# Performance work log

Measured on AMD Instinct MI355X. Metric: run time of the kernel, lower is better.

Reference implementation:

```python
import jax, jax.numpy as jnp
import numpy as np

N, T, F, H, NH, OUT = 4096, 32, 7, 64, 8, 8


def setup_inputs() -> dict:
    key = jax.random.key(0)
    ks = jax.random.split(key, 24)
    def nrm(k, shape, scale):
        return jax.random.normal(k, shape, jnp.float32) * scale
    s_gru = 1.0 / np.sqrt(H)
    s_gat = 1.0 / np.sqrt(NH * OUT)
    s_lin = 0.05
    return {
        "inputs": jax.random.normal(ks[0], (N, T, F), jnp.float32),
        "adj": jax.random.randint(ks[1], (N, N), 0, 2, jnp.int32),
        "W_ih": nrm(ks[2], (3 * H, F), s_gru),
        "W_hh": nrm(ks[3], (3 * H, H), s_gru),
        "b_ih": nrm(ks[4], (3 * H,), s_gru),
        "b_hh": nrm(ks[5], (3 * H,), s_gru),
        "gat_w": nrm(ks[6], (H, NH * OUT), s_gat),
        "gat_wu": nrm(ks[7], (NH, OUT, 1), 1.0),
        "gat_wv": nrm(ks[8], (NH, OUT, 1), 1.0),
        "gat_bias": nrm(ks[9], (1, NH * OUT), s_gat),
        "proj_w": nrm(ks[10], (NH * OUT, H), s_lin),
        "proj_b": nrm(ks[11], (NH * OUT,), s_lin),
        "mlp_self_w": nrm(ks[12], (H, H), s_lin),
        "mlp_self_b": nrm(ks[13], (H,), s_lin),
        "mlp_pos_w": nrm(ks[14], (H, NH * OUT), s_lin),
        "mlp_pos_b": nrm(ks[15], (H,), s_lin),
        "sem_w1": nrm(ks[16], (H, H), s_lin),
        "sem_b1": nrm(ks[17], (H,), s_lin),
        "sem_w2": nrm(ks[18], (1, H), s_lin),
        "pred_w": nrm(ks[19], (1, H), s_lin),
        "pred_b": nrm(ks[20], (1,), s_lin),
    }


def reference(inputs, adj, W_ih, W_hh, b_ih, b_hh, gat_w, gat_wu, gat_wv,
              gat_bias, proj_w, proj_b, mlp_self_w, mlp_self_b,
              mlp_pos_w, mlp_pos_b, sem_w1, sem_b1, sem_w2, pred_w, pred_b):
    n = inputs.shape[0]
    # --- GRU encoder (batch_first, 1 layer); take final hidden state ---
    gx = jnp.einsum('ntf,gf->tng', inputs, W_ih) + b_ih  # [T, N, 3H]
    h0 = jnp.zeros((n, W_hh.shape[1]), inputs.dtype)

    def step(h, g):
        gh = h @ W_hh.T + b_hh
        gxr, gxz, gxn = jnp.split(g, 3, axis=-1)
        ghr, ghz, ghn = jnp.split(gh, 3, axis=-1)
        r = jax.nn.sigmoid(gxr + ghr)
        z = jax.nn.sigmoid(gxz + ghz)
        nn_ = jnp.tanh(gxn + r * ghn)
        return (1.0 - z) * nn_ + z * h, None

    h, _ = jax.lax.scan(step, h0, gx)  # [N, H]

    # --- multi-head GAT over dense adjacency ---
    sup = (h @ gat_w).reshape(n, NH, OUT).transpose(1, 0, 2)  # [nh, N, out]
    f1 = jnp.einsum('hnd,hdo->hn', sup, gat_wu)[:, None, :]   # [nh, 1, N]
    f2 = jnp.einsum('hnd,hdo->hn', sup, gat_wv)[:, :, None]   # [nh, N, 1]
    logits = jax.nn.leaky_relu(f1 + f2, negative_slope=0.2)   # [nh, N, N]
    adjf = adj.astype(logits.dtype)[None]                     # [1, N, N]
    mw = logits * adjf
    ex = jnp.exp(mw - jnp.max(mw, axis=2, keepdims=True)) * (adjf > 0)
    attn = ex / jnp.clip(jnp.sum(ex, axis=2, keepdims=True), 1e-10)
    pos = jnp.einsum('hij,hjd->hid', attn, sup)               # [nh, N, out]
    pos = pos.transpose(1, 0, 2).reshape(n, NH * OUT)
    pos = pos + gat_bias + h @ proj_w.T + proj_b              # bias + residual proj

    # --- stack self/pos channels, PairNorm (mode='PN') ---
    s = jnp.stack([h @ mlp_self_w.T + mlp_self_b,
                   pos @ mlp_pos_w.T + mlp_pos_b], axis=1)    # [N, 2, H]
    s = s - s.mean(axis=0)
    rownorm_mean = jnp.sqrt(1e-6 + jnp.mean(jnp.sum(s * s, axis=1)))
    s = s / rownorm_mean

    # --- semantic attention over the 2 channels ---
    w = jnp.tanh(s @ sem_w1.T + sem_b1) @ sem_w2.T            # [N, 2, 1]
    we = jnp.exp(w - jnp.max(w, axis=1, keepdims=True))
    beta = we / (jnp.sum(we, axis=1, keepdims=True) + 1e-10)
    emb = jnp.sum(beta * s, axis=1)                           # [N, H]

    # --- predictor ---
    return jax.nn.sigmoid(emb @ pred_w.T + pred_b)            # [N, 1]
```

## Files before the change

kernel.cpp:

```cpp
#include <hip/hip_runtime.h>
#include <math.h>

#define NN 4096
#define TT 32
#define FF 7
#define HH 64
#define NHEAD 8
#define DOUT 8
#define LOG2E 1.44269504f

#if __has_builtin(__builtin_amdgcn_exp2f)
#define EXP2(x) __builtin_amdgcn_exp2f(x)
#else
#define EXP2(x) exp2f(x)
#endif

typedef short bf16x8 __attribute__((ext_vector_type(8)));
typedef float f32x4 __attribute__((ext_vector_type(4)));

__device__ __forceinline__ float sigm(float x){
  x = fminf(fmaxf(x, -30.f), 30.f);
  return 1.f / (1.f + __expf(-x));
}
__device__ __forceinline__ float tanh_fast(float x){
  x = fminf(fmaxf(x, -15.f), 15.f);
  float e = __expf(2.f*x);
  return (e - 1.f) / (e + 1.f);
}
__device__ __forceinline__ unsigned short bf16rne(float f){
  unsigned u = __float_as_uint(f);
  u += 0x7fffu + ((u >> 16) & 1u);
  return (unsigned short)(u >> 16);
}
__device__ __forceinline__ unsigned bfpack2(float a, float b){
  return (unsigned)bf16rne(a) | ((unsigned)bf16rne(b) << 16);
}
__device__ __forceinline__ unsigned cvtpk_bf16(float a, float b){
  unsigned r;
  asm("v_cvt_pk_bf16_f32 %0, %1, %2" : "=v"(r) : "v"(a), "v"(b));
  return r;
}

__global__ __launch_bounds__(256) void k0_prep(
    const float* __restrict__ pw, const float* __restrict__ msw,
    const float* __restrict__ mpw, const float* __restrict__ sw1,
    const float* __restrict__ Wih, const float* __restrict__ Whh,
    const float* __restrict__ bih, const float* __restrict__ bhh,
    float* __restrict__ wtproj, float* __restrict__ wtself,
    float* __restrict__ wtpos, float* __restrict__ wtsem,
    uint4* __restrict__ whhF, uint4* __restrict__ wihF)
{
  if (blockIdx.x < 16){
    int tid = threadIdx.x + blockIdx.x*256;
    int d = tid >> 6, k = tid & 63;
    wtproj[k*64+d] = pw[tid];
    wtself[k*64+d] = msw[tid];
    wtpos[k*64+d]  = mpw[tid];
    wtsem[k*64+d]  = sw1[tid];
    return;
  }
  int idx = (blockIdx.x-16)*256 + threadIdx.x;
  if (idx < 24*64){
    int f = idx >> 6, lane = idx & 63;
    int T = f >> 1, c = f & 1;
    int g = T*16 + (lane & 15);
    const float* wp = Whh + g*64 + c*32 + (lane >> 4)*8;
    uint4 v;
    v.x = bfpack2(wp[0], wp[1]);
    v.y = bfpack2(wp[2], wp[3]);
    v.z = bfpack2(wp[4], wp[5]);
    v.w = bfpack2(wp[6], wp[7]);
    whhF[idx] = v;
  } else if (idx < 36*64){
    int i2 = idx - 24*64;
    int T = i2 >> 6, lane = i2 & 63;
    int g = T*16 + (lane & 15);
    int kg = lane >> 4;
    float bias = (T < 8) ? (bih[g] + bhh[g]) : bih[g];
    float f8[8];
    #pragma unroll
    for (int j = 0; j < 8; ++j){
      int k = kg*8 + j;
      f8[j] = (k < 7) ? Wih[g*7 + k] : ((k == 7) ? bias : 0.f);
    }
    uint4 v;
    v.x = bfpack2(f8[0], f8[1]); v.y = bfpack2(f8[2], f8[3]);
    v.z = bfpack2(f8[4], f8[5]); v.w = bfpack2(f8[6], f8[7]);
    wihF[i2] = v;
  }
}

__global__ __launch_bounds__(256) void k1_gru(
    const float* __restrict__ x,
    const uint4* __restrict__ whhF,
    const uint4* __restrict__ wihF,
    const float* __restrict__ bhh,
    float* __restrict__ hout)
{
  __shared__ __align__(16) short s_xb[32][16][8];
  __shared__ __align__(16) short s_hb[2][16][72];

  int tid = threadIdx.x;
  int lane = tid & 63, w = tid >> 6;
  int nb = blockIdx.x * 16;
  int row = lane & 15;
  int kg  = lane >> 4;

  union U { bf16x8 v; uint4 q; };
  U u;
  u.q = wihF[w*64 + lane];           bf16x8 fRx  = u.v;
  u.q = whhF[(w*2+0)*64 + lane];     bf16x8 fRh0 = u.v;
  u.q = whhF[(w*2+1)*64 + lane];     bf16x8 fRh1 = u.v;
  u.q = wihF[(4+w)*64 + lane];       bf16x8 fZx  = u.v;
  u.q = whhF[((4+w)*2+0)*64 + lane]; bf16x8 fZh0 = u.v;
  u.q = whhF[((4+w)*2+1)*64 + lane]; bf16x8 fZh1 = u.v;
  u.q = wihF[(8+w)*64 + lane];       bf16x8 fNx  = u.v;
  u.q = whhF[((8+w)*2+0)*64 + lane]; bf16x8 fNh0 = u.v;
  u.q = whhF[((8+w)*2+1)*64 + lane]; bf16x8 fNh1 = u.v;

  for (int s = tid; s < 4096; s += 256){
    int t = s >> 7, node = (s >> 3) & 15, k = s & 7;
    float v = (k < 7) ? x[(size_t)(nb + node)*224 + t*7 + k] : ((k == 7) ? 1.f : 0.f);
    s_xb[t][node][k] = (short)bf16rne(v);
  }
  for (int i = tid; i < 576; i += 256) ((unsigned*)&s_hb[0][0][0])[i] = 0u;

  float bhn_[4];
  #pragma unroll
  for (int j = 0; j < 4; ++j) bhn_[j] = bhh[128 + w*16 + kg*4 + j];
  float hreg[4] = {0.f, 0.f, 0.f, 0.f};
  f32x4 z4 = {0.f, 0.f, 0.f, 0.f};

  __syncthreads();
  int cur = 0;
  for (int t = 0; t < TT; ++t){
    bf16x8 bx = {0,0,0,0,0,0,0,0};
    if (lane < 16) bx = *(const bf16x8*)&s_xb[t][row][0];
    bf16x8 bh0 = *(const bf16x8*)&s_hb[cur][row][kg*8];
    bf16x8 bh1 = *(const bf16x8*)&s_hb[cur][row][32 + kg*8];

    f32x4 aR = __builtin_amdgcn_mfma_f32_16x16x32_bf16(fRx, bx, z4, 0, 0, 0);
    aR = __builtin_amdgcn_mfma_f32_16x16x32_bf16(fRh0, bh0, aR, 0, 0, 0);
    aR = __builtin_amdgcn_mfma_f32_16x16x32_bf16(fRh1, bh1, aR, 0, 0, 0);
    f32x4 aZ = __builtin_amdgcn_mfma_f32_16x16x32_bf16(fZx, bx, z4, 0, 0, 0);
    aZ = __builtin_amdgcn_mfma_f32_16x16x32_bf16(fZh0, bh0, aZ, 0, 0, 0);
    aZ = __builtin_amdgcn_mfma_f32_16x16x32_bf16(fZh1, bh1, aZ, 0, 0, 0);
    f32x4 aNx = __builtin_amdgcn_mfma_f32_16x16x32_bf16(fNx, bx, z4, 0, 0, 0);
    f32x4 aNh = __builtin_amdgcn_mfma_f32_16x16x32_bf16(fNh0, bh0, z4, 0, 0, 0);
    aNh = __builtin_amdgcn_mfma_f32_16x16x32_bf16(fNh1, bh1, aNh, 0, 0, 0);

    #pragma unroll
    for (int j = 0; j < 4; ++j){
      float rr = sigm(aR[j]);
      float zz = sigm(aZ[j]);
      float nn = tanh_fast(aNx[j] + rr*(aNh[j] + bhn_[j]));
      hreg[j] = (1.f - zz)*nn + zz*hreg[j];
    }
    uint2 p;
    p.x = bfpack2(hreg[0], hreg[1]);
    p.y = bfpack2(hreg[2], hreg[3]);
    *(uint2*)&s_hb[cur^1][row][w*16 + kg*4] = p;
    __syncthreads();
    cur ^= 1;
  }

  #pragma unroll
  for (int j = 0; j < 4; ++j)
    hout[(size_t)(nb + row)*64 + w*16 + kg*4 + j] = hreg[j];
}

__global__ __launch_bounds__(256) void k2_sup(
    const float* __restrict__ h, const float* __restrict__ gat_w,
    const float* __restrict__ wu, const float* __restrict__ wv,
    unsigned short* __restrict__ supbJ,
    float* __restrict__ f1t,
    float* __restrict__ f2)
{
  int tid = threadIdx.x;
  int wave = tid >> 6, lane = tid & 63;
  int n = blockIdx.x*4 + wave;
  float hreg = h[n*64 + lane];
  float acc = 0.f;
  #pragma unroll
  for (int k = 0; k < 64; ++k){
    float hk = __shfl(hreg, k, 64);
    acc += hk * gat_w[k*64 + lane];
  }
  int hh = lane >> 3, o = lane & 7;
  supbJ[(size_t)hh*32768 + (n>>3)*64 + o*8 + (n&7)] = bf16rne(acc);
  float p1 = acc * wu[lane];
  float p2 = acc * wv[lane];
  #pragma unroll
  for (int s = 1; s < 8; s <<= 1){
    p1 += __shfl_xor(p1, s, 64);
    p2 += __shfl_xor(p2, s, 64);
  }
  if (o == 0){
    f1t[(size_t)hh*NN + n] = p1 * LOG2E;
    f2[n*8 + hh] = p2 * LOG2E;
  }
}

__global__ __launch_bounds__(256) void k2c_pack(const int* __restrict__ adj,
                                               unsigned long long* __restrict__ adjmT)
{
  int lane = threadIdx.x & 63, wave = threadIdx.x >> 6;
  int row = blockIdx.x*4 + wave;
  const int* ap = adj + (size_t)row*NN;
  size_t base = (size_t)(row >> 4)*1024 + (row & 15);
  #pragma unroll 8
  for (int s = 0; s < 64; ++s){
    unsigned long long m = __ballot(ap[s*64 + lane] != 0);
    if (lane == 0) adjmT[base + s*16] = m;
  }
}

__global__ __launch_bounds__(256) void k3_gat(
    const unsigned long long* __restrict__ adjmT,
    const unsigned short* __restrict__ supbJ,
    const float* __restrict__ f1t,
    const float* __restrict__ f2,
    float* __restrict__ posg)
{
  __shared__ f32x4 s_acc[4][64];
  int tid = threadIdx.x;
  int lane = tid & 63, js = tid >> 6;
  int gid = blockIdx.x;
  int ib = gid >> 3, h = gid & 7;
  int i0 = ib*16;
  int col = lane & 15;
  int kg  = lane >> 4;

  float f2v = f2[(size_t)(i0+col)*8 + h];

  const unsigned long long* mrowT = adjmT + (size_t)ib*1024;
  const float* f1p = f1t + (size_t)h*NN;
  const unsigned short* bsrcJ = supbJ + (size_t)h*32768;
  unsigned bge8 = (col >= 8) ? 0xffffffffu : 0u;

  f32x4 acc = {0.f, 0.f, 0.f, 0.f};

  #pragma unroll 4
  for (int cc = 0; cc < 32; ++cc){
    int c = js*32 + cc;
    int j8 = c*32 + kg*8;
    unsigned long long mw = mrowT[(c >> 1)*16 + col];
    unsigned mb = (unsigned)(mw >> (((c & 1) << 5) + (kg << 3)));
    float4 fa = *(const float4*)(f1p + j8);
    float4 fb = *(const float4*)(f1p + j8 + 4);

    float p[8];
    p[0]=fa.x; p[1]=fa.y; p[2]=fa.z; p[3]=fa.w;
    p[4]=fb.x; p[5]=fb.y; p[6]=fb.z; p[7]=fb.w;
    #pragma unroll
    for (int e = 0; e < 8; ++e){
      float ls = p[e] + f2v;
      float lrs = fmaxf(ls, 0.2f*ls);
      float pe = EXP2(lrs);
      p[e] = (mb & (1u << e)) ? pe : 0.f;
    }
    union { bf16x8 v; unsigned u[4]; } A;
    A.u[0] = cvtpk_bf16(p[0], p[1]);
    A.u[1] = cvtpk_bf16(p[2], p[3]);
    A.u[2] = cvtpk_bf16(p[4], p[5]);
    A.u[3] = cvtpk_bf16(p[6], p[7]);

    union { bf16x8 v; unsigned u[4]; } B;
    uint4 ld = *(const uint4*)(bsrcJ + (size_t)(c*4 + kg)*64 + (col & 7)*8);
    B.u[0] = bge8 ? 0x3f803f80u : ld.x;
    B.u[1] = bge8 ? 0x3f803f80u : ld.y;
    B.u[2] = bge8 ? 0x3f803f80u : ld.z;
    B.u[3] = bge8 ? 0x3f803f80u : ld.w;

    acc = __builtin_amdgcn_mfma_f32_16x16x32_bf16(A.v, B.v, acc, 0, 0, 0);
  }

  s_acc[js][lane] = acc;
  __syncthreads();
  if (js == 0){
    f32x4 a1 = s_acc[1][lane], a2 = s_acc[2][lane], a3 = s_acc[3][lane];
    #pragma unroll
    for (int j = 0; j < 4; ++j) acc[j] += a1[j] + a2[j] + a3[j];

    int slane = (lane & 48) + 8;
    #pragma unroll
    for (int r4 = 0; r4 < 4; ++r4){
      float sv = __shfl(acc[r4], slane, 64);
      float inv = 1.f / fmaxf(sv, 1e-10f);
      if (col < 8)
        posg[(size_t)(i0 + kg*4 + r4)*64 + h*8 + col] = acc[r4] * inv;
    }
  }
}

__global__ __launch_bounds__(256) void k4_mix(
    const float* __restrict__ h, const float* __restrict__ posg,
    const float* __restrict__ gat_bias, const float* __restrict__ proj_b,
    const float* __restrict__ wtproj, const float* __restrict__ wtself,
    const float* __restrict__ wtpos,
    const float* __restrict__ mlp_self_b, const float* __restrict__ mlp_pos_b,
    float* __restrict__ s0, float* __restrict__ s1, float* __restrict__ part)
{
  int tid = threadIdx.x;
  int wave = tid >> 6, lane = tid & 63;
  int n = blockIdx.x*4 + wave;
  float hreg = h[n*64 + lane];
  float pr = proj_b[lane];
  float se = mlp_self_b[lane];
  #pragma unroll
  for (int k = 0; k < 64; ++k){
    float hk = __shfl(hreg, k, 64);
    pr += hk * wtproj[k*64 + lane];
    se += hk * wtself[k*64 + lane];
  }
  float posf = posg[n*64 + lane] + gat_bias[lane] + pr;
  float s1v = mlp_pos_b[lane];
  #pragma unroll
  for (int k = 0; k < 64; ++k){
    float pk = __shfl(posf, k, 64);
    s1v += pk * wtpos[k*64 + lane];
  }
  s0[n*64+lane] = se;
  s1[n*64+lane] = s1v;

  __shared__ float sb0[4][64];
  __shared__ float sb1[4][64];
  __shared__ float sq[4];
  sb0[wave][lane] = se;
  sb1[wave][lane] = s1v;
  float q = se*se + s1v*s1v;
  #pragma unroll
  for (int s = 1; s < 64; s <<= 1) q += __shfl_xor(q, s, 64);
  if (lane == 0) sq[wave] = q;
  __syncthreads();
  if (tid < 64){
    part[blockIdx.x*130 + tid] = sb0[0][tid]+sb0[1][tid]+sb0[2][tid]+sb0[3][tid];
  } else if (tid < 128){
    int d = tid - 64;
    part[blockIdx.x*130 + 64 + d] = sb1[0][d]+sb1[1][d]+sb1[2][d]+sb1[3][d];
  } else if (tid == 128){
    part[blockIdx.x*130 + 128] = sq[0]+sq[1]+sq[2]+sq[3];
  }
}

__global__ __launch_bounds__(1024) void k5_stats(const float* __restrict__ part, float* __restrict__ stats)
{
  int tid = threadIdx.x;
  __shared__ float s_mu[8][128];
  __shared__ float s_sq[8];
  int c = tid & 127, ch = tid >> 7;
  float a = 0.f;
  for (int b = ch*128; b < ch*128+128; ++b) a += part[b*130 + c];
  s_mu[ch][c] = a;
  if (tid < 8){
    float q = 0.f;
    for (int b = tid*128; b < tid*128+128; ++b) q += part[b*130 + 128];
    s_sq[tid] = q;
  }
  __syncthreads();
  if (tid < 128){
    float m = 0.f;
    #pragma unroll
    for (int j = 0; j < 8; ++j) m += s_mu[j][tid];
    s_mu[0][tid] = m;
    stats[tid] = m / 4096.f;
  }
  __syncthreads();
  if (tid == 0){
    float sq = 0.f;
    #pragma unroll
    for (int j = 0; j < 8; ++j) sq += s_sq[j];
    float mu2 = 0.f;
    for (int i = 0; i < 128; ++i){ float m = s_mu[0][i] / 4096.f; mu2 += m*m; }
    float msq = sq/(4096.f*64.f) - mu2/64.f;
    stats[128] = 1.f / sqrtf(1e-6f + msq);
  }
}

__global__ __launch_bounds__(256) void k6_sem(
    const float* __restrict__ s0, const float* __restrict__ s1,
    const float* __restrict__ stats, const float* __restrict__ wtsem,
    const float* __restrict__ sem_b1, const float* __restrict__ sem_w2,
    const float* __restrict__ pred_w, const float* __restrict__ pred_b,
    float* __restrict__ out)
{
  int tid = threadIdx.x;
  int wave = tid >> 6, lane = tid & 63;
  int n = blockIdx.x*4 + wave;
  float rinv = stats[128];
  float a0 = (s0[n*64+lane] - stats[lane]) * rinv;
  float a1 = (s1[n*64+lane] - stats[64+lane]) * rinv;
  float t0 = sem_b1[lane], t1 = t0;
  #pragma unroll
  for (int k = 0; k < 64; ++k){
    float w = wtsem[k*64 + lane];
    t0 += __shfl(a0, k, 64) * w;
    t1 += __shfl(a1, k, 64) * w;
  }
  t0 = tanh_fast(t0); t1 = tanh_fast(t1);
  float w2 = sem_w2[lane];
  float w0 = t0*w2, w1 = t1*w2;
  #pragma unroll
  for (int s = 1; s < 64; s <<= 1){
    w0 += __shfl_xor(w0, s, 64);
    w1 += __shfl_xor(w1, s, 64);
  }
  float mx = fmaxf(w0, w1);
  float e0 = __expf(w0 - mx), e1 = __expf(w1 - mx);
  float denom = e0 + e1 + 1e-10f;
  float b0 = e0/denom, b1 = e1/denom;
  float emb = b0*a0 + b1*a1;
  float pl = emb * pred_w[lane];
  #pragma unroll
  for (int s = 1; s < 64; s <<= 1) pl += __shfl_xor(pl, s, 64);
  if (lane == 0) out[n] = sigm(pl + pred_b[0]);
}

extern "C" void kernel_launch(void* const* d_in, const int* in_sizes, int n_in,
                              void* d_out, int out_size, void* d_ws, size_t ws_size,
                              hipStream_t stream)
{
  (void)in_sizes; (void)n_in; (void)out_size; (void)ws_size;
  const float* x         = (const float*)d_in[0];
  const int*   adj       = (const int*)d_in[1];
  const float* W_ih      = (const float*)d_in[2];
  const float* W_hh      = (const float*)d_in[3];
  const float* b_ih      = (const float*)d_in[4];
  const float* b_hh      = (const float*)d_in[5];
  const float* gat_w     = (const float*)d_in[6];
  const float* gat_wu    = (const float*)d_in[7];
  const float* gat_wv    = (const float*)d_in[8];
  const float* gat_bias  = (const float*)d_in[9];
  const float* proj_w    = (const float*)d_in[10];
  const float* proj_b    = (const float*)d_in[11];
  const float* mlp_self_w= (const float*)d_in[12];
  const float* mlp_self_b= (const float*)d_in[13];
  const float* mlp_pos_w = (const float*)d_in[14];
  const float* mlp_pos_b = (const float*)d_in[15];
  const float* sem_w1    = (const float*)d_in[16];
  const float* sem_b1    = (const float*)d_in[17];
  const float* sem_w2    = (const float*)d_in[18];
  const float* pred_w    = (const float*)d_in[19];
  const float* pred_b    = (const float*)d_in[20];
  float* out = (float*)d_out;
  float* ws  = (float*)d_ws;

  float* h     = ws + 0;
  unsigned short* supbJ = (unsigned short*)(ws + 262144);
  float* f1t   = ws + 524288;
  float* f2    = ws + 557056;
  float* posg  = ws + 589824;
  float* s0    = ws + 851968;
  float* s1    = ws + 1114112;
  unsigned long long* adjmT = (unsigned long long*)(ws + 851968);
  uint4* whhF = (uint4*)(ws + 1114112 + 200000);
  uint4* wihF = whhF + 24*64;
  float* part  = ws + 1376256;
  float* stats = ws + 1517576;
  float* wtproj= ws + 1517712;
  float* wtself= wtproj + 4096;
  float* wtpos = wtself + 4096;
  float* wtsem = wtpos  + 4096;

  k0_prep<<<25, 256, 0, stream>>>(proj_w, mlp_self_w, mlp_pos_w, sem_w1,
                                  W_ih, W_hh, b_ih, b_hh,
                                  wtproj, wtself, wtpos, wtsem, whhF, wihF);
  k1_gru<<<256, 256, 0, stream>>>(x, whhF, wihF, b_hh, h);
  k2_sup<<<1024, 256, 0, stream>>>(h, gat_w, gat_wu, gat_wv, supbJ, f1t, f2);
  k2c_pack<<<1024, 256, 0, stream>>>(adj, adjmT);
  k3_gat<<<2048, 256, 0, stream>>>(adjmT, supbJ, f1t, f2, posg);
  k4_mix<<<1024, 256, 0, stream>>>(h, posg, gat_bias, proj_b, wtproj, wtself, wtpos,
                                   mlp_self_b, mlp_pos_b, s0, s1, part);
  k5_stats<<<1, 1024, 0, stream>>>(part, stats);
  k6_sem<<<1024, 256, 0, stream>>>(s0, s1, stats, wtsem, sem_b1, sem_w2, pred_w, pred_b, out);
}
```

Measured before the change: 165.2 us.

## Factor GAT exponentials, shrink GRU blocks to 4 nodes, load ones tile from memory

The GAT inner loop no longer evaluates exp2 per edge. The per-source factors exp2(f1) and exp2(0.2*f1) are computed once in k2_sup, and the per-row factors once per lane, so each edge costs a compare, two selects and a multiply. The sign test of the leaky-relu argument is done against exp2(-f2), and the product of two exponentials can overflow or lose precision differently from a single exp2. The GRU kernel now processes 4 nodes per block over 1024 blocks instead of 16 nodes over 256, which raises parallelism but wastes 12 of 16 MFMA rows. The constant-ones B operand is now read from a small buffer filled by k0_prep instead of being selected per element.

```diff
diff --git a/kernel.cpp b/kernel.cpp
--- a/kernel.cpp
+++ b/kernel.cpp
@@ -48,7 +48,8 @@
     const float* __restrict__ bih, const float* __restrict__ bhh,
     float* __restrict__ wtproj, float* __restrict__ wtself,
     float* __restrict__ wtpos, float* __restrict__ wtsem,
-    uint4* __restrict__ whhF, uint4* __restrict__ wihF)
+    uint4* __restrict__ whhF, uint4* __restrict__ wihF,
+    unsigned* __restrict__ onesb)
 {
   if (blockIdx.x < 16){
     int tid = threadIdx.x + blockIdx.x*256;
@@ -59,6 +60,7 @@
     wtsem[k*64+d]  = sw1[tid];
     return;
   }
+  if (blockIdx.x == 16 && threadIdx.x < 32) onesb[threadIdx.x] = 0x3f803f80u;
   int idx = (blockIdx.x-16)*256 + threadIdx.x;
   if (idx < 24*64){
     int f = idx >> 6, lane = idx & 63;
@@ -97,12 +99,12 @@
     const float* __restrict__ bhh,
     float* __restrict__ hout)
 {
-  __shared__ __align__(16) short s_xb[32][16][8];
-  __shared__ __align__(16) short s_hb[2][16][72];
+  __shared__ __align__(16) short s_xb[32][4][8];
+  __shared__ __align__(16) short s_hb[2][4][72];
 
   int tid = threadIdx.x;
   int lane = tid & 63, w = tid >> 6;
-  int nb = blockIdx.x * 16;
+  int nb = blockIdx.x * 4;
   int row = lane & 15;
   int kg  = lane >> 4;
 
@@ -118,12 +120,12 @@
   u.q = whhF[((8+w)*2+0)*64 + lane]; bf16x8 fNh0 = u.v;
   u.q = whhF[((8+w)*2+1)*64 + lane]; bf16x8 fNh1 = u.v;
 
-  for (int s = tid; s < 4096; s += 256){
-    int t = s >> 7, node = (s >> 3) & 15, k = s & 7;
+  for (int s = tid; s < 1024; s += 256){
+    int t = s >> 5, node = (s >> 3) & 3, k = s & 7;
     float v = (k < 7) ? x[(size_t)(nb + node)*224 + t*7 + k] : ((k == 7) ? 1.f : 0.f);
     s_xb[t][node][k] = (short)bf16rne(v);
   }
-  for (int i = tid; i < 576; i += 256) ((unsigned*)&s_hb[0][0][0])[i] = 0u;
+  for (int i = tid; i < 288; i += 256) ((unsigned*)&s_hb[0][0][0])[i] = 0u;
 
   float bhn_[4];
   #pragma unroll
@@ -133,11 +135,12 @@
 
   __syncthreads();
   int cur = 0;
+  int nrow = row & 3;
   for (int t = 0; t < TT; ++t){
     bf16x8 bx = {0,0,0,0,0,0,0,0};
-    if (lane < 16) bx = *(const bf16x8*)&s_xb[t][row][0];
-    bf16x8 bh0 = *(const bf16x8*)&s_hb[cur][row][kg*8];
-    bf16x8 bh1 = *(const bf16x8*)&s_hb[cur][row][32 + kg*8];
+    if (lane < 16) bx = *(const bf16x8*)&s_xb[t][nrow][0];
+    bf16x8 bh0 = *(const bf16x8*)&s_hb[cur][nrow][kg*8];
+    bf16x8 bh1 = *(const bf16x8*)&s_hb[cur][nrow][32 + kg*8];
 
     f32x4 aR = __builtin_amdgcn_mfma_f32_16x16x32_bf16(fRx, bx, z4, 0, 0, 0);
     aR = __builtin_amdgcn_mfma_f32_16x16x32_bf16(fRh0, bh0, aR, 0, 0, 0);
@@ -156,24 +159,28 @@
       float nn = tanh_fast(aNx[j] + rr*(aNh[j] + bhn_[j]));
       hreg[j] = (1.f - zz)*nn + zz*hreg[j];
     }
-    uint2 p;
-    p.x = bfpack2(hreg[0], hreg[1]);
-    p.y = bfpack2(hreg[2], hreg[3]);
-    *(uint2*)&s_hb[cur^1][row][w*16 + kg*4] = p;
+    if (row < 4){
+      uint2 p;
+      p.x = bfpack2(hreg[0], hreg[1]);
+      p.y = bfpack2(hreg[2], hreg[3]);
+      *(uint2*)&s_hb[cur^1][row][w*16 + kg*4] = p;
+    }
     __syncthreads();
     cur ^= 1;
   }
 
-  #pragma unroll
-  for (int j = 0; j < 4; ++j)
-    hout[(size_t)(nb + row)*64 + w*16 + kg*4 + j] = hreg[j];
+  if (row < 4){
+    #pragma unroll
+    for (int j = 0; j < 4; ++j)
+      hout[(size_t)(nb + row)*64 + w*16 + kg*4 + j] = hreg[j];
+  }
 }
 
 __global__ __launch_bounds__(256) void k2_sup(
     const float* __restrict__ h, const float* __restrict__ gat_w,
     const float* __restrict__ wu, const float* __restrict__ wv,
     unsigned short* __restrict__ supbJ,
-    float* __restrict__ f1t,
+    float2* __restrict__ e1t,
     float* __restrict__ f2)
 {
   int tid = threadIdx.x;
@@ -196,7 +203,8 @@
     p2 += __shfl_xor(p2, s, 64);
   }
   if (o == 0){
-    f1t[(size_t)hh*NN + n] = p1 * LOG2E;
+    float p1s = p1 * LOG2E;
+    e1t[(size_t)hh*NN + n] = make_float2(EXP2(p1s), EXP2(0.2f*p1s));
     f2[n*8 + hh] = p2 * LOG2E;
   }
 }
@@ -218,8 +226,9 @@
 __global__ __launch_bounds__(256) void k3_gat(
     const unsigned long long* __restrict__ adjmT,
     const unsigned short* __restrict__ supbJ,
-    const float* __restrict__ f1t,
+    const float2* __restrict__ e1t,
     const float* __restrict__ f2,
+    const unsigned short* __restrict__ onesb,
     float* __restrict__ posg)
 {
   __shared__ f32x4 s_acc[4][64];
@@ -231,12 +240,16 @@
   int col = lane & 15;
   int kg  = lane >> 4;
 
-  float f2v = f2[(size_t)(i0+col)*8 + h];
+  float f2s = f2[(size_t)(i0+col)*8 + h];
+  float E2  = EXP2(f2s);
+  float E2s = EXP2(0.2f*f2s);
+  float T   = EXP2(-f2s);
 
   const unsigned long long* mrowT = adjmT + (size_t)ib*1024;
-  const float* f1p = f1t + (size_t)h*NN;
-  const unsigned short* bsrcJ = supbJ + (size_t)h*32768;
-  unsigned bge8 = (col >= 8) ? 0xffffffffu : 0u;
+  const float2* e1p = e1t + (size_t)h*NN;
+  int bge8 = (col >= 8);
+  const unsigned short* bbase = bge8 ? onesb
+                                     : (supbJ + (size_t)h*32768 + (col & 7)*8);
 
   f32x4 acc = {0.f, 0.f, 0.f, 0.f};
 
@@ -246,17 +259,18 @@
     int j8 = c*32 + kg*8;
     unsigned long long mw = mrowT[(c >> 1)*16 + col];
     unsigned mb = (unsigned)(mw >> (((c & 1) << 5) + (kg << 3)));
-    float4 fa = *(const float4*)(f1p + j8);
-    float4 fb = *(const float4*)(f1p + j8 + 4);
-
+    const float4* ep = (const float4*)(e1p + j8);
+    float4 qa = ep[0], qb = ep[1], qc = ep[2], qd = ep[3];
+
+    float e1v[8]  = {qa.x, qa.z, qb.x, qb.z, qc.x, qc.z, qd.x, qd.z};
+    float e1sv[8] = {qa.y, qa.w, qb.y, qb.w, qc.y, qc.w, qd.y, qd.w};
     float p[8];
-    p[0]=fa.x; p[1]=fa.y; p[2]=fa.z; p[3]=fa.w;
-    p[4]=fb.x; p[5]=fb.y; p[6]=fb.z; p[7]=fb.w;
     #pragma unroll
     for (int e = 0; e < 8; ++e){
-      float ls = p[e] + f2v;
-      float lrs = fmaxf(ls, 0.2f*ls);
-      float pe = EXP2(lrs);
+      bool pos = e1v[e] > T;
+      float m1 = pos ? e1v[e] : e1sv[e];
+      float m2 = pos ? E2 : E2s;
+      float pe = m1 * m2;
       p[e] = (mb & (1u << e)) ? pe : 0.f;
     }
     union { bf16x8 v; unsigned u[4]; } A;
@@ -265,12 +279,9 @@
     A.u[2] = cvtpk_bf16(p[4], p[5]);
     A.u[3] = cvtpk_bf16(p[6], p[7]);
 
-    union { bf16x8 v; unsigned u[4]; } B;
-    uint4 ld = *(const uint4*)(bsrcJ + (size_t)(c*4 + kg)*64 + (col & 7)*8);
-    B.u[0] = bge8 ? 0x3f803f80u : ld.x;
-    B.u[1] = bge8 ? 0x3f803f80u : ld.y;
-    B.u[2] = bge8 ? 0x3f803f80u : ld.z;
-    B.u[3] = bge8 ? 0x3f803f80u : ld.w;
+    int boff = bge8 ? 0 : ((c*4 + kg) << 6);
+    union { bf16x8 v; uint4 q; } B;
+    B.q = *(const uint4*)(bbase + boff);
 
     acc = __builtin_amdgcn_mfma_f32_16x16x32_bf16(A.v, B.v, acc, 0, 0, 0);
   }
@@ -447,8 +458,9 @@
 
   float* h     = ws + 0;
   unsigned short* supbJ = (unsigned short*)(ws + 262144);
-  float* f1t   = ws + 524288;
-  float* f2    = ws + 557056;
+  float2* e1t  = (float2*)(ws + 393216);
+  float* f2    = ws + 458752;
+  unsigned* onesb = (unsigned*)(ws + 524288);
   float* posg  = ws + 589824;
   float* s0    = ws + 851968;
   float* s1    = ws + 1114112;
@@ -464,11 +476,11 @@
 
   k0_prep<<<25, 256, 0, stream>>>(proj_w, mlp_self_w, mlp_pos_w, sem_w1,
                                   W_ih, W_hh, b_ih, b_hh,
-                                  wtproj, wtself, wtpos, wtsem, whhF, wihF);
-  k1_gru<<<256, 256, 0, stream>>>(x, whhF, wihF, b_hh, h);
-  k2_sup<<<1024, 256, 0, stream>>>(h, gat_w, gat_wu, gat_wv, supbJ, f1t, f2);
+                                  wtproj, wtself, wtpos, wtsem, whhF, wihF, onesb);
+  k1_gru<<<1024, 256, 0, stream>>>(x, whhF, wihF, b_hh, h);
+  k2_sup<<<1024, 256, 0, stream>>>(h, gat_w, gat_wu, gat_wv, supbJ, e1t, f2);
   k2c_pack<<<1024, 256, 0, stream>>>(adj, adjmT);
-  k3_gat<<<2048, 256, 0, stream>>>(adjmT, supbJ, f1t, f2, posg);
+  k3_gat<<<2048, 256, 0, stream>>>(adjmT, supbJ, e1t, f2, (const unsigned short*)onesb, posg);
   k4_mix<<<1024, 256, 0, stream>>>(h, posg, gat_bias, proj_b, wtproj, wtself, wtpos,
                                    mlp_self_b, mlp_pos_b, s0, s1, part);
   k5_stats<<<1, 1024, 0, stream>>>(part, stats);
```

After: 217.3 us. 31.5% more time.
